# Kernel optimization log

Measured on AMD Instinct MI355X. Metric: run time of the kernel, lower is better.

Reference implementation:

```python
import jax, jax.numpy as jnp
import numpy as np


def setup_inputs() -> dict:
    key = jax.random.key(0)
    kq, kk, kv = jax.random.split(key, 3)
    B, H, S, D = 2, 16, 2048, 64
    Q = jax.random.normal(kq, (B, H, S, D), dtype=jnp.float32)
    K = jax.random.normal(kk, (B, H, S, D), dtype=jnp.float32)
    V = jax.random.normal(kv, (B, H, S, D), dtype=jnp.float32)
    return {"Q": Q, "K": K, "V": V}


def reference(Q, K, V):
    # Faithful to the torch module: NO 1/sqrt(d_k) scaling (d_k is computed
    # but never used in the original forward).
    scores = jnp.einsum('bhqd,bhkd->bhqk', Q, K)      # [B,H,S,S]
    attn = jax.nn.softmax(scores, axis=-1)
    out = jnp.einsum('bhqk,bhkd->bhqd', attn, V)      # [B,H,S,D]
    return out
```

## Files before the change

### kernel.cpp

```cpp
#include <hip/hip_runtime.h>


typedef __bf16    bf16_t;
typedef _Float16  f16_t;
typedef __bf16    bf16x8 __attribute__((ext_vector_type(8)));
typedef _Float16  f16x8  __attribute__((ext_vector_type(8)));
typedef float     f32x4  __attribute__((ext_vector_type(4)));

constexpr int S  = 2048;
constexpr int Dh = 64;
constexpr int KT = 64;
constexpr int QT = 128;
constexpr float LOG2E = 1.44269504088896340736f;

__device__ __forceinline__ int sw(int row, int col) {
    return row * 64 + ((((col >> 3) ^ (row & 7)) << 3) | (col & 7));
}

template<bool SPLIT>
__global__ __launch_bounds__(256, 4)
void attn_kernel(const float* __restrict__ Qg,
                 const float* __restrict__ Kg,
                 const float* __restrict__ Vg,
                 float* __restrict__ Og,
                 float* __restrict__ Opart,
                 float* __restrict__ lpart)
{
    __shared__ alignas(16) f16_t  Khs[KT * Dh];
    __shared__ alignas(16) bf16_t Vts[Dh * KT];
    __shared__ alignas(16) bf16_t Pbs[QT * Dh];

    const int tid  = threadIdx.x;
    const int lane = tid & 63;
    const int wv   = tid >> 6;
    const int l15  = lane & 15;
    const int qd   = lane >> 4;
    const int wb   = wv * 32;

    const int bx   = blockIdx.x;
    const int head = bx & 31;
    const int r5   = bx >> 5;
    const int qt   = SPLIT ? (r5 >> 1) : r5;
    const int half = SPLIT ? (r5 & 1) : 0;
    const int tile = head * 16 + qt;
    const int ch0  = SPLIT ? half * 16 : 0;
    const int nch  = SPLIT ? 16 : 32;

    const float* Qp = Qg + (size_t)tile * QT * Dh;
    const float* Kp = Kg + (size_t)head * S * Dh;
    const float* Vp = Vg + (size_t)head * S * Dh;

    const int skey = tid >> 4;
    const int sc4  = (tid & 15) * 4;
    const int vkb  = (tid & 15) * 4;
    const int vc4  = (tid >> 4) * 4;

    f16x8 qf[2][2];
    #pragma unroll
    for (int sub = 0; sub < 2; ++sub) {
        const float* qrow = Qp + (size_t)(wb + sub * 16 + l15) * Dh;
        #pragma unroll
        for (int ks = 0; ks < 2; ++ks) {
            const float* p = qrow + ks * 32 + qd * 8;
            const float4 a = *(const float4*)(p);
            const float4 b = *(const float4*)(p + 4);
            const float xs[8] = {a.x, a.y, a.z, a.w, b.x, b.y, b.z, b.w};
            #pragma unroll
            for (int j = 0; j < 8; ++j) qf[sub][ks][j] = (f16_t)(xs[j] * LOG2E);
        }
    }

    f32x4 oa[2][4];
    float lp[2];
    #pragma unroll
    for (int s2 = 0; s2 < 2; ++s2) {
        lp[s2] = 0.f;
        #pragma unroll
        for (int t = 0; t < 4; ++t) oa[s2][t] = (f32x4){0.f, 0.f, 0.f, 0.f};
    }

    float4 kbuf[4], vbuf[4];
    {
        const float* Kc = Kp + (size_t)ch0 * KT * Dh;
        const float* Vc = Vp + (size_t)ch0 * KT * Dh;
        #pragma unroll
        for (int it = 0; it < 4; ++it)
            kbuf[it] = *(const float4*)(Kc + (size_t)(it * 16 + skey) * Dh + sc4);
        #pragma unroll
        for (int i = 0; i < 4; ++i)
            vbuf[i] = *(const float4*)(Vc + (size_t)(vkb + i) * Dh + vc4);
    }

    #pragma unroll 1
    for (int ci = 0; ci < nch; ++ci) {
        __syncthreads();

        #pragma unroll
        for (int it = 0; it < 4; ++it) {
            const float xs[4] = {kbuf[it].x, kbuf[it].y, kbuf[it].z, kbuf[it].w};
            union { f16_t h[4]; uint2 u; } ph;
            #pragma unroll
            for (int j = 0; j < 4; ++j) ph.h[j] = (f16_t)xs[j];
            *(uint2*)&Khs[sw(it * 16 + skey, sc4)] = ph.u;
        }
        {
            const float rs[4][4] = {{vbuf[0].x, vbuf[1].x, vbuf[2].x, vbuf[3].x},
                                    {vbuf[0].y, vbuf[1].y, vbuf[2].y, vbuf[3].y},
                                    {vbuf[0].z, vbuf[1].z, vbuf[2].z, vbuf[3].z},
                                    {vbuf[0].w, vbuf[1].w, vbuf[2].w, vbuf[3].w}};
            #pragma unroll
            for (int i = 0; i < 4; ++i) {
                union { bf16_t h[4]; uint2 u; } pv;
                #pragma unroll
                for (int j = 0; j < 4; ++j) pv.h[j] = (bf16_t)rs[i][j];
                *(uint2*)&Vts[sw(vc4 + i, vkb)] = pv.u;
            }
        }
        __syncthreads();

        if (ci + 1 < nch) {
            const float* Kc = Kp + (size_t)(ch0 + ci + 1) * KT * Dh;
            const float* Vc = Vp + (size_t)(ch0 + ci + 1) * KT * Dh;
            #pragma unroll
            for (int it = 0; it < 4; ++it)
                kbuf[it] = *(const float4*)(Kc + (size_t)(it * 16 + skey) * Dh + sc4);
            #pragma unroll
            for (int i = 0; i < 4; ++i)
                vbuf[i] = *(const float4*)(Vc + (size_t)(vkb + i) * Dh + vc4);
        }

        #pragma unroll
        for (int np = 0; np < 2; ++np) {
            f32x4 st[2][2];
            #pragma unroll
            for (int s2 = 0; s2 < 2; ++s2)
                #pragma unroll
                for (int t = 0; t < 2; ++t) st[s2][t] = (f32x4){0.f, 0.f, 0.f, 0.f};
            __builtin_amdgcn_s_setprio(1);
            #pragma unroll
            for (int ks = 0; ks < 2; ++ks) {
                const int co = ks * 32 + qd * 8;
                const f16x8 ak0 = *(const f16x8*)&Khs[sw((np * 2 + 0) * 16 + l15, co)];
                const f16x8 ak1 = *(const f16x8*)&Khs[sw((np * 2 + 1) * 16 + l15, co)];
                #pragma unroll
                for (int s2 = 0; s2 < 2; ++s2) {
                    st[s2][0] = __builtin_amdgcn_mfma_f32_16x16x32_f16(ak0, qf[s2][ks], st[s2][0], 0, 0, 0);
                    st[s2][1] = __builtin_amdgcn_mfma_f32_16x16x32_f16(ak1, qf[s2][ks], st[s2][1], 0, 0, 0);
                }
            }
            __builtin_amdgcn_s_setprio(0);
            #pragma unroll
            for (int s2 = 0; s2 < 2; ++s2) {
                #pragma unroll
                for (int t = 0; t < 2; ++t) {
                    union { bf16_t h[4]; uint2 u; } pb;
                    #pragma unroll
                    for (int r = 0; r < 4; ++r) {
                        const float e = __builtin_amdgcn_exp2f(st[s2][t][r]);
                        lp[s2] += e;
                        pb.h[r] = (bf16_t)e;
                    }
                    *(uint2*)&Pbs[sw(wb + s2 * 16 + l15, (np * 2 + t) * 16 + qd * 4)] = pb.u;
                }
            }
        }

        __builtin_amdgcn_s_setprio(1);
        #pragma unroll
        for (int ks = 0; ks < 2; ++ks) {
            const int co = ks * 32 + qd * 8;
            const bf16x8 pa0 = *(const bf16x8*)&Pbs[sw(wb + l15,      co)];
            const bf16x8 pa1 = *(const bf16x8*)&Pbs[sw(wb + 16 + l15, co)];
            #pragma unroll
            for (int dt = 0; dt < 4; ++dt) {
                const bf16x8 vb = *(const bf16x8*)&Vts[sw(dt * 16 + l15, co)];
                oa[0][dt] = __builtin_amdgcn_mfma_f32_16x16x32_bf16(pa0, vb, oa[0][dt], 0, 0, 0);
                oa[1][dt] = __builtin_amdgcn_mfma_f32_16x16x32_bf16(pa1, vb, oa[1][dt], 0, 0, 0);
            }
        }
        __builtin_amdgcn_s_setprio(0);
    }

    #pragma unroll
    for (int s2 = 0; s2 < 2; ++s2) {
        lp[s2] += __shfl_xor(lp[s2], 16, 64);
        lp[s2] += __shfl_xor(lp[s2], 32, 64);
    }

    if (SPLIT) {
        float* Po = Opart + (size_t)(tile * 2 + half) * (QT * Dh);
        float* lq = lpart + (size_t)(tile * 2 + half) * QT;
        #pragma unroll
        for (int s2 = 0; s2 < 2; ++s2) {
            if (qd == 0) lq[wb + s2 * 16 + l15] = lp[s2];
            #pragma unroll
            for (int r = 0; r < 4; ++r) {
                const int row = wb + s2 * 16 + qd * 4 + r;
                #pragma unroll
                for (int dt = 0; dt < 4; ++dt)
                    Po[(size_t)row * Dh + dt * 16 + l15] = oa[s2][dt][r];
            }
        }
    } else {
        float* Op = Og + (size_t)tile * QT * Dh;
        #pragma unroll
        for (int s2 = 0; s2 < 2; ++s2) {
            #pragma unroll
            for (int r = 0; r < 4; ++r) {
                const float inv = 1.0f / __shfl(lp[s2], qd * 4 + r, 64);
                const int row = wb + s2 * 16 + qd * 4 + r;
                #pragma unroll
                for (int dt = 0; dt < 4; ++dt)
                    Op[(size_t)row * Dh + dt * 16 + l15] = oa[s2][dt][r] * inv;
            }
        }
    }
}

__global__ __launch_bounds__(256)
void combine_kernel(const float* __restrict__ Opart,
                    const float* __restrict__ lpart,
                    float* __restrict__ Og)
{
    const int i  = blockIdx.x * 256 + threadIdx.x;
    const int q  = i >> 11;
    const int rw = (i >> 4) & 127;
    const size_t e = (size_t)(i & 2047) * 4;
    const float4 a = *(const float4*)(Opart + (size_t)(2 * q)     * (QT * Dh) + e);
    const float4 b = *(const float4*)(Opart + (size_t)(2 * q + 1) * (QT * Dh) + e);
    const float  l = lpart[(size_t)(2 * q) * QT + rw] + lpart[(size_t)(2 * q + 1) * QT + rw];
    const float inv = 1.0f / l;
    float4 o;
    o.x = (a.x + b.x) * inv;
    o.y = (a.y + b.y) * inv;
    o.z = (a.z + b.z) * inv;
    o.w = (a.w + b.w) * inv;
    *(float4*)(Og + (size_t)i * 4) = o;
}

extern "C" void kernel_launch(void* const* d_in, const int* in_sizes, int n_in,
                              void* d_out, int out_size, void* d_ws, size_t ws_size,
                              hipStream_t stream)
{
    const float* Q = (const float*)d_in[0];
    const float* K = (const float*)d_in[1];
    const float* V = (const float*)d_in[2];
    float*       O = (float*)d_out;

    constexpr size_t NPART       = 1024;
    constexpr size_t OPART_ELEMS = NPART * QT * Dh;
    constexpr size_t LPART_ELEMS = NPART * QT;
    constexpr size_t NEED = (OPART_ELEMS + LPART_ELEMS) * sizeof(float);

    if (ws_size >= NEED) {
        float* Opart = (float*)d_ws;
        float* lpart = Opart + OPART_ELEMS;
        attn_kernel<true><<<dim3(1024), dim3(256), 0, stream>>>(
            Q, K, V, nullptr, Opart, lpart);
        const int n4 = (int)(OPART_ELEMS / 2 / 4);
        combine_kernel<<<dim3(n4 / 256), dim3(256), 0, stream>>>(Opart, lpart, O);
    } else {
        attn_kernel<false><<<dim3(512), dim3(256), 0, stream>>>(
            Q, K, V, O, nullptr, nullptr);
    }
}
```

Before: 155.5 us.

## Split KV into three chunks, shrink P buffer, raise occupancy to six blocks

```diff
diff --git a/kernel.cpp b/kernel.cpp
--- a/kernel.cpp
+++ b/kernel.cpp
@@ -17,8 +17,12 @@
     return row * 64 + ((((col >> 3) ^ (row & 7)) << 3) | (col & 7));
 }
 
-template<bool SPLIT>
-__global__ __launch_bounds__(256, 4)
+__device__ __forceinline__ int swp(int row, int k) {
+    return sw(row >> 1, (row & 1) * 32 + k);
+}
+
+template<int SN>
+__global__ __launch_bounds__(256, 6)
 void attn_kernel(const float* __restrict__ Qg,
                  const float* __restrict__ Kg,
                  const float* __restrict__ Vg,
@@ -28,7 +32,7 @@
 {
     __shared__ alignas(16) f16_t  Khs[KT * Dh];
     __shared__ alignas(16) bf16_t Vts[Dh * KT];
-    __shared__ alignas(16) bf16_t Pbs[QT * Dh];
+    __shared__ alignas(16) bf16_t Pbs[64 * 64];
 
     const int tid  = threadIdx.x;
     const int lane = tid & 63;
@@ -40,11 +44,11 @@
     const int bx   = blockIdx.x;
     const int head = bx & 31;
     const int r5   = bx >> 5;
-    const int qt   = SPLIT ? (r5 >> 1) : r5;
-    const int half = SPLIT ? (r5 & 1) : 0;
+    const int qt   = r5 / SN;
+    const int half = r5 % SN;
     const int tile = head * 16 + qt;
-    const int ch0  = SPLIT ? half * 16 : 0;
-    const int nch  = SPLIT ? 16 : 32;
+    const int ch0  = (SN == 3) ? half * 11 : half * 16;
+    const int nch  = (SN == 3) ? (half == 2 ? 10 : 11) : (SN == 2 ? 16 : 32);
 
     const float* Qp = Qg + (size_t)tile * QT * Dh;
     const float* Kp = Kg + (size_t)head * S * Dh;
@@ -52,8 +56,8 @@
 
     const int skey = tid >> 4;
     const int sc4  = (tid & 15) * 4;
-    const int vkb  = (tid & 15) * 4;
-    const int vc4  = (tid >> 4) * 4;
+    const int vkb  = (tid >> 4) * 4;
+    const int vc4  = (tid & 15) * 4;
 
     f16x8 qf[2][2];
     #pragma unroll
@@ -160,25 +164,21 @@
                         lp[s2] += e;
                         pb.h[r] = (bf16_t)e;
                     }
-                    *(uint2*)&Pbs[sw(wb + s2 * 16 + l15, (np * 2 + t) * 16 + qd * 4)] = pb.u;
+                    *(uint2*)&Pbs[swp(wb + s2 * 16 + l15, t * 16 + qd * 4)] = pb.u;
                 }
             }
-        }
-
-        __builtin_amdgcn_s_setprio(1);
-        #pragma unroll
-        for (int ks = 0; ks < 2; ++ks) {
-            const int co = ks * 32 + qd * 8;
-            const bf16x8 pa0 = *(const bf16x8*)&Pbs[sw(wb + l15,      co)];
-            const bf16x8 pa1 = *(const bf16x8*)&Pbs[sw(wb + 16 + l15, co)];
+            const int co = np * 32 + qd * 8;
+            const bf16x8 pa0 = *(const bf16x8*)&Pbs[swp(wb + l15,      qd * 8)];
+            const bf16x8 pa1 = *(const bf16x8*)&Pbs[swp(wb + 16 + l15, qd * 8)];
+            __builtin_amdgcn_s_setprio(1);
             #pragma unroll
             for (int dt = 0; dt < 4; ++dt) {
                 const bf16x8 vb = *(const bf16x8*)&Vts[sw(dt * 16 + l15, co)];
                 oa[0][dt] = __builtin_amdgcn_mfma_f32_16x16x32_bf16(pa0, vb, oa[0][dt], 0, 0, 0);
                 oa[1][dt] = __builtin_amdgcn_mfma_f32_16x16x32_bf16(pa1, vb, oa[1][dt], 0, 0, 0);
             }
-        }
-        __builtin_amdgcn_s_setprio(0);
+            __builtin_amdgcn_s_setprio(0);
+        }
     }
 
     #pragma unroll
@@ -187,9 +187,9 @@
         lp[s2] += __shfl_xor(lp[s2], 32, 64);
     }
 
-    if (SPLIT) {
-        float* Po = Opart + (size_t)(tile * 2 + half) * (QT * Dh);
-        float* lq = lpart + (size_t)(tile * 2 + half) * QT;
+    if (SN > 1) {
+        float* Po = Opart + (size_t)(tile * SN + half) * (QT * Dh);
+        float* lq = lpart + (size_t)(tile * SN + half) * QT;
         #pragma unroll
         for (int s2 = 0; s2 < 2; ++s2) {
             if (qd == 0) lq[wb + s2 * 16 + l15] = lp[s2];
@@ -217,6 +217,7 @@
     }
 }
 
+template<int SN>
 __global__ __launch_bounds__(256)
 void combine_kernel(const float* __restrict__ Opart,
                     const float* __restrict__ lpart,
@@ -226,15 +227,17 @@
     const int q  = i >> 11;
     const int rw = (i >> 4) & 127;
     const size_t e = (size_t)(i & 2047) * 4;
-    const float4 a = *(const float4*)(Opart + (size_t)(2 * q)     * (QT * Dh) + e);
-    const float4 b = *(const float4*)(Opart + (size_t)(2 * q + 1) * (QT * Dh) + e);
-    const float  l = lpart[(size_t)(2 * q) * QT + rw] + lpart[(size_t)(2 * q + 1) * QT + rw];
+    float4 acc = {0.f, 0.f, 0.f, 0.f};
+    float  l   = 0.f;
+    #pragma unroll
+    for (int h = 0; h < SN; ++h) {
+        const float4 a = *(const float4*)(Opart + (size_t)(q * SN + h) * (QT * Dh) + e);
+        l += lpart[(size_t)(q * SN + h) * QT + rw];
+        acc.x += a.x; acc.y += a.y; acc.z += a.z; acc.w += a.w;
+    }
     const float inv = 1.0f / l;
     float4 o;
-    o.x = (a.x + b.x) * inv;
-    o.y = (a.y + b.y) * inv;
-    o.z = (a.z + b.z) * inv;
-    o.w = (a.w + b.w) * inv;
+    o.x = acc.x * inv; o.y = acc.y * inv; o.z = acc.z * inv; o.w = acc.w * inv;
     *(float4*)(Og + (size_t)i * 4) = o;
 }
 
@@ -247,20 +250,25 @@
     const float* V = (const float*)d_in[2];
     float*       O = (float*)d_out;
 
-    constexpr size_t NPART       = 1024;
-    constexpr size_t OPART_ELEMS = NPART * QT * Dh;
-    constexpr size_t LPART_ELEMS = NPART * QT;
-    constexpr size_t NEED = (OPART_ELEMS + LPART_ELEMS) * sizeof(float);
-
-    if (ws_size >= NEED) {
+    constexpr size_t TILE_O = (size_t)QT * Dh;
+    constexpr size_t NEED3  = (512ull * 3 * (TILE_O + QT)) * sizeof(float);
+    constexpr size_t NEED2  = (512ull * 2 * (TILE_O + QT)) * sizeof(float);
+    const int n4 = (int)(512 * TILE_O / 4);
+
+    if (ws_size >= NEED3) {
         float* Opart = (float*)d_ws;
-        float* lpart = Opart + OPART_ELEMS;
-        attn_kernel<true><<<dim3(1024), dim3(256), 0, stream>>>(
+        float* lpart = Opart + 512ull * 3 * TILE_O;
+        attn_kernel<3><<<dim3(1536), dim3(256), 0, stream>>>(
             Q, K, V, nullptr, Opart, lpart);
-        const int n4 = (int)(OPART_ELEMS / 2 / 4);
-        combine_kernel<<<dim3(n4 / 256), dim3(256), 0, stream>>>(Opart, lpart, O);
+        combine_kernel<3><<<dim3(n4 / 256), dim3(256), 0, stream>>>(Opart, lpart, O);
+    } else if (ws_size >= NEED2) {
+        float* Opart = (float*)d_ws;
+        float* lpart = Opart + 512ull * 2 * TILE_O;
+        attn_kernel<2><<<dim3(1024), dim3(256), 0, stream>>>(
+            Q, K, V, nullptr, Opart, lpart);
+        combine_kernel<2><<<dim3(n4 / 256), dim3(256), 0, stream>>>(Opart, lpart, O);
     } else {
-        attn_kernel<false><<<dim3(512), dim3(256), 0, stream>>>(
+        attn_kernel<1><<<dim3(512), dim3(256), 0, stream>>>(
             Q, K, V, O, nullptr, nullptr);
     }
 }
```

Result: slower. 388.1 us (+149.6%).
